# Optimization experiments

Hardware: AMD Instinct MI355X
Metric: run time of the kernel (lower is better)

The kernel has to match this reference:

```python
import jax, jax.numpy as jnp
import numpy as np

N, D, IN, HID, OUT, E = 20000, 8, 64, 128, 64, 100000
EPS = 1e-5


def _bn(h, g, b):
    # training-mode BatchNorm1d: biased batch variance, eps=1e-5
    m = h.mean(axis=0)
    v = jnp.mean((h - m) ** 2, axis=0)
    return (h - m) * jax.lax.rsqrt(v + EPS) * g + b


def setup_inputs() -> dict:
    key = jax.random.key(0)
    ks = jax.random.split(key, 12)
    x = jax.random.normal(ks[0], (N, IN), dtype=jnp.float32)
    node_ts = jax.random.uniform(ks[1], (N,), dtype=jnp.float32)
    neighbor_idx = jax.random.randint(ks[2], (N, D), 0, N, dtype=jnp.int32)
    neighbor_ts = jax.random.uniform(ks[3], (N, D), dtype=jnp.float32)
    target = jax.random.randint(ks[4], (2, E), 0, N, dtype=jnp.int32)
    neg_pairs = jax.random.randint(ks[5], (2, E), 0, N, dtype=jnp.int32)
    W1 = jax.random.normal(ks[6], (IN, HID), dtype=jnp.float32) * (1.0 / np.sqrt(IN))
    b1 = jnp.zeros((HID,), jnp.float32)
    g1 = jnp.ones((HID,), jnp.float32)
    be1 = jnp.zeros((HID,), jnp.float32)
    W2 = jax.random.normal(ks[7], (HID, OUT), dtype=jnp.float32) * (1.0 / np.sqrt(HID))
    b2 = jnp.zeros((OUT,), jnp.float32)
    g2 = jnp.ones((OUT,), jnp.float32)
    be2 = jnp.zeros((OUT,), jnp.float32)
    Wd = jax.random.normal(ks[8], (OUT, 1), dtype=jnp.float32) * (1.0 / np.sqrt(OUT))
    bd = jnp.zeros((1,), jnp.float32)
    return {"x": x, "node_ts": node_ts, "neighbor_idx": neighbor_idx,
            "neighbor_ts": neighbor_ts, "target": target, "neg_pairs": neg_pairs,
            "W1": W1, "b1": b1, "g1": g1, "be1": be1,
            "W2": W2, "b2": b2, "g2": g2, "be2": be2, "Wd": Wd, "bd": bd}


def reference(x, node_ts, neighbor_idx, neighbor_ts, target, neg_pairs,
              W1, b1, g1, be1, W2, b2, g2, be2, Wd, bd):
    n = jnp.arange(N, dtype=neighbor_idx.dtype)
    # ---- level-2 queries: every node at its own timestamp ----
    # children = D temporal-neighbor slots + self (self always valid, ts=node_ts)
    c_idx = jnp.concatenate([neighbor_idx, n[:, None]], axis=1)          # [N, D+1]
    c_ts = jnp.concatenate([neighbor_ts, node_ts[:, None]], axis=1)      # [N, D+1]
    mask2 = jnp.concatenate([neighbor_ts <= node_ts[:, None],
                             jnp.ones((N, 1), bool)], axis=1)            # [N, D+1]
    # ---- level-1 queries: each (child node, child ts) pair ----
    ci = c_idx.reshape(-1)                                               # [M]
    cts = c_ts.reshape(-1)
    gc_idx = jnp.concatenate([neighbor_idx[ci], ci[:, None]], axis=1)    # [M, D+1]
    mask1 = jnp.concatenate([neighbor_ts[ci] <= cts[:, None],
                             jnp.ones((ci.shape[0], 1), bool)], axis=1)
    # ---- layer 0: raw features of grandchildren ----
    h0 = x[gc_idx]                                                       # [M, D+1, IN]
    m1 = mask1.astype(x.dtype)
    agg1 = jnp.einsum('mk,mkf->mf', m1, h0) / m1.sum(1, keepdims=True)   # masked mean
    h1 = jax.nn.relu(_bn(agg1 @ W1 + b1, g1, be1))                       # [M, HID]
    h1 = h1.reshape(N, D + 1, HID)
    # ---- layer 2 aggregation over temporal children ----
    m2 = mask2.astype(x.dtype)
    agg2 = jnp.einsum('nk,nkf->nf', m2, h1) / m2.sum(1, keepdims=True)
    embs = jax.nn.relu(_bn(agg2 @ W2 + b2, g2, be2))                     # [N, OUT]
    # ---- HadNet link decoder + BCEWithLogits ----
    pos = (embs[target[0]] * embs[target[1]]) @ Wd + bd                  # [E, 1]
    neg = (embs[neg_pairs[0]] * embs[neg_pairs[1]]) @ Wd + bd            # [E, 1]
    preds = jnp.concatenate([pos, neg], axis=0)[:, 0]                    # [2E]
    labels = jnp.concatenate([jnp.ones((E,), x.dtype), jnp.zeros((E,), x.dtype)])
    loss = jnp.mean(jnp.maximum(preds, 0.0) - preds * labels
                    + jnp.log1p(jnp.exp(-jnp.abs(preds))))
    return loss
```

## Files before the change

kernel.cpp:

```cpp
#include <hip/hip_runtime.h>
#include <math.h>

constexpr int kN = 20000;
constexpr int kD = 8;
constexpr int kE = 100000;
constexpr int kM = kN * 9;
constexpr int kTiles1 = kM / 16;
constexpr int kTiles3 = kN / 16;
constexpr int kGroups = kN / 16;
constexpr float kEps = 1e-5f;

constexpr int S_SUM1 = 0, S_SQ1 = 128, S_SUM2 = 256, S_SQ2 = 320;

constexpr size_t OFF_MEANP = 23040000;
constexpr size_t OFF_AGG2  = 23040000;
constexpr size_t OFF_PRE2  = 28160000;
constexpr size_t OFF_EMBS  = 33280000;
constexpr size_t OFF_EMBSW = 38400000;
constexpr size_t OFF_STATS = 43520000;

typedef short short8 __attribute__((ext_vector_type(8)));
typedef float floatx4 __attribute__((ext_vector_type(4)));

__device__ __forceinline__ unsigned f2bf(float f) {
  unsigned u = __float_as_uint(f);
  u += 0x7fffu + ((u >> 16) & 1u);
  return u >> 16;
}

__global__ __launch_bounds__(256) void k0_prefix(
    const float* __restrict__ x, const int* __restrict__ nidx,
    const float* __restrict__ nts, unsigned short* __restrict__ meanp,
    float* __restrict__ stats)
{
  if (blockIdx.x == 0 && threadIdx.x < 384) stats[threadIdx.x] = 0.f;
  const int c = blockIdx.x * 4 + (threadIdx.x >> 6);
  const int lane = threadIdx.x & 63;

  float tsv[8]; int idxv[8];
#pragma unroll
  for (int j = 0; j < 8; ++j) {
    tsv[j] = nts[c * 8 + j];
    idxv[j] = nidx[c * 8 + j];
  }
  int rank[8];
#pragma unroll
  for (int j = 0; j < 8; ++j) {
    int r = 0;
#pragma unroll
    for (int j2 = 0; j2 < 8; ++j2)
      r += (tsv[j2] < tsv[j] || (tsv[j2] == tsv[j] && j2 < j)) ? 1 : 0;
    rank[j] = r;
  }
  int ord[8];
#pragma unroll
  for (int k = 0; k < 8; ++k) {
    int js = 0;
#pragma unroll
    for (int j = 0; j < 8; ++j) if (rank[j] == k) js = j;
    ord[k] = idxv[js];
  }

  float acc = x[c * 64 + lane];
  unsigned short* mp = meanp + (size_t)c * 576 + lane;
  mp[0] = (unsigned short)f2bf(acc);
#pragma unroll
  for (int k = 0; k < 8; ++k) {
    acc += x[ord[k] * 64 + lane];
    mp[(k + 1) * 64] = (unsigned short)f2bf(acc / (float)(k + 2));
  }
}

__global__ __launch_bounds__(256) void kB_rows(
    const float* __restrict__ node_ts, const int* __restrict__ nidx,
    const float* __restrict__ nts, const unsigned short* __restrict__ meanp,
    unsigned short* __restrict__ agg1)
{
  const int n = blockIdx.x * 4 + (threadIdx.x >> 6);
  const int lane = threadIdx.x & 63;
  const float tn = node_ts[n];
  const int g = lane >> 3, jj = lane & 7;
#pragma unroll
  for (int s = 0; s < 9; ++s) {
    int c; float t;
    if (s < 8) { c = nidx[n * 8 + s]; t = nts[n * 8 + s]; }
    else       { c = n;               t = tn; }
    int rank = 0;
#pragma unroll
    for (int j = 0; j < 8; ++j) rank += (nts[c * 8 + j] <= t) ? 1 : 0;
    unsigned short v = meanp[(size_t)c * 576 + rank * 64 + lane];
    int m = n * 9 + s;
    int tt = m >> 4, r = m & 15;
    agg1[tt * 1024 + g * 128 + r * 8 + jj] = v;
  }
}

__global__ __launch_bounds__(256, 3) void k1s_stats(
    const unsigned short* __restrict__ aggA,
    const float* __restrict__ W1, const float* __restrict__ b1,
    float* __restrict__ stats)
{
  __shared__ unsigned short W1T[128 * 72];
  __shared__ float redS[256][8];
  __shared__ float redQ[256][8];

  const int tid = threadIdx.x;
  const int lane = tid & 63;
  const int wave = tid >> 6;
  const int l15 = lane & 15;
  const int q = lane >> 4;

  for (int i = tid; i < 8192; i += 256) {
    int n = i >> 6, k = i & 63;
    W1T[n * 72 + k] = (unsigned short)f2bf(W1[k * 128 + n]);
  }
  __syncthreads();

  short8 bf[8][2];
#pragma unroll
  for (int c = 0; c < 8; ++c)
#pragma unroll
    for (int s = 0; s < 2; ++s)
      bf[c][s] = *(const short8*)&W1T[(c * 16 + l15) * 72 + q * 8 + s * 32];

  float b1c[8];
#pragma unroll
  for (int c = 0; c < 8; ++c) b1c[c] = b1[c * 16 + l15];

  float sum8[8], sq8[8];
#pragma unroll
  for (int c = 0; c < 8; ++c) { sum8[c] = 0.f; sq8[c] = 0.f; }

  const int gw = blockIdx.x * 4 + wave;
  const int nw = gridDim.x * 4;

  for (int t = gw; t < kTiles1; t += nw) {
    const unsigned short* ap = aggA + (size_t)t * 1024;
    short8 af0 = *(const short8*)(ap + q * 128 + l15 * 8);
    short8 af1 = *(const short8*)(ap + (4 + q) * 128 + l15 * 8);

    floatx4 acc[8];
#pragma unroll
    for (int c = 0; c < 8; ++c) {
      acc[c] = (floatx4){0.f, 0.f, 0.f, 0.f};
      acc[c] = __builtin_amdgcn_mfma_f32_16x16x32_bf16(af0, bf[c][0], acc[c], 0, 0, 0);
      acc[c] = __builtin_amdgcn_mfma_f32_16x16x32_bf16(af1, bf[c][1], acc[c], 0, 0, 0);
    }
#pragma unroll
    for (int c = 0; c < 8; ++c)
#pragma unroll
      for (int i = 0; i < 4; ++i) {
        float v = acc[c][i] + b1c[c];
        sum8[c] += v; sq8[c] += v * v;
      }
  }

  __syncthreads();
#pragma unroll
  for (int c = 0; c < 8; ++c) { redS[tid][c] = sum8[c]; redQ[tid][c] = sq8[c]; }
  __syncthreads();
  if (tid < 128) {
    int c = tid >> 4, r15 = tid & 15;
    float s = 0.f, qq = 0.f;
#pragma unroll
    for (int w = 0; w < 4; ++w)
#pragma unroll
      for (int p = 0; p < 4; ++p) {
        int T = w * 64 + p * 16 + r15;
        s += redS[T][c]; qq += redQ[T][c];
      }
    atomicAdd(&stats[S_SUM1 + tid], s);
    atomicAdd(&stats[S_SQ1 + tid], qq);
  }
}

__global__ __launch_bounds__(256, 2) void k2_apply(
    const unsigned short* __restrict__ aggA, const float* __restrict__ node_ts,
    const float* __restrict__ nts, const float* __restrict__ W1,
    const float* __restrict__ b1, const float* __restrict__ g1,
    const float* __restrict__ be1, const float* __restrict__ stats,
    unsigned* __restrict__ agg2dw)
{
  __shared__ unsigned short W1T[128 * 72];
  __shared__ unsigned short H[144 * 128];
  __shared__ float sc[128], sh[128];
  __shared__ float wbuf[144];
  __shared__ float rvs[16];

  const int tid = threadIdx.x;
  const int lane = tid & 63;
  const int wave = tid >> 6;
  const int l15 = lane & 15;
  const int q = lane >> 4;
  const int g = blockIdx.x;
  const int n0 = g * 16;

  for (int i = tid; i < 8192; i += 256) {
    int n = i >> 6, k = i & 63;
    W1T[n * 72 + k] = (unsigned short)f2bf(W1[k * 128 + n]);
  }
  if (tid < 128) {
    float mean = stats[S_SUM1 + tid] * (1.f / kM);
    float var  = stats[S_SQ1 + tid] * (1.f / kM) - mean * mean;
    float s    = g1[tid] * rsqrtf(var + kEps);
    sc[tid] = s; sh[tid] = be1[tid] - mean * s;
  }
  if (tid < 144) {
    int nd = n0 + tid / 9, slot = tid % 9;
    wbuf[tid] = (slot < kD) ? ((nts[nd * kD + slot] <= node_ts[nd]) ? 1.f : 0.f)
                            : 1.f;
  }
  __syncthreads();

  short8 bfr[8][2];
#pragma unroll
  for (int c = 0; c < 8; ++c)
#pragma unroll
    for (int s = 0; s < 2; ++s)
      bfr[c][s] = *(const short8*)&W1T[(c * 16 + l15) * 72 + q * 8 + s * 32];

  float scc[8], shc[8];
#pragma unroll
  for (int c = 0; c < 8; ++c) {
    int col = c * 16 + l15;
    scc[c] = sc[col];
    shc[c] = fmaf(b1[col], sc[col], sh[col]);
  }
  if (tid < 16) {
    float s = 0.f;
#pragma unroll
    for (int j = 0; j < 9; ++j) s += wbuf[tid * 9 + j];
    rvs[tid] = 1.f / s;
  }

  for (int t9 = wave; t9 < 9; t9 += 4) {
    const unsigned short* ap = aggA + (size_t)(g * 9 + t9) * 1024;
    short8 af0 = *(const short8*)(ap + q * 128 + l15 * 8);
    short8 af1 = *(const short8*)(ap + (4 + q) * 128 + l15 * 8);

    floatx4 acc[8];
#pragma unroll
    for (int c = 0; c < 8; ++c) {
      acc[c] = (floatx4){0.f, 0.f, 0.f, 0.f};
      acc[c] = __builtin_amdgcn_mfma_f32_16x16x32_bf16(af0, bfr[c][0], acc[c], 0, 0, 0);
      acc[c] = __builtin_amdgcn_mfma_f32_16x16x32_bf16(af1, bfr[c][1], acc[c], 0, 0, 0);
    }
#pragma unroll
    for (int i = 0; i < 4; ++i) {
      int lr = t9 * 16 + q * 4 + i;
#pragma unroll
      for (int c = 0; c < 8; ++c) {
        int col = c * 16 + l15;
        float h = fmaxf(fmaf(acc[c][i], scc[c], shc[c]), 0.f);
        H[lr * 128 + col] = (unsigned short)f2bf(h);
      }
    }
  }
  __syncthreads();

  const unsigned* Hdw = (const unsigned*)H;
#pragma unroll
  for (int j = 0; j < 4; ++j) {
    int ndl = 4 * wave + j;
    float s0 = 0.f, s1 = 0.f;
#pragma unroll
    for (int slot = 0; slot < 9; ++slot) {
      int lr = ndl * 9 + slot;
      float w = wbuf[lr];
      unsigned u = Hdw[lr * 64 + lane];
      s0 = fmaf(w, __uint_as_float(u << 16), s0);
      s1 = fmaf(w, __uint_as_float(u & 0xffff0000u), s1);
    }
    float r = rvs[ndl];
    agg2dw[(size_t)(n0 + ndl) * 64 + lane] =
        f2bf(s0 * r) | (f2bf(s1 * r) << 16);
  }
}

__global__ __launch_bounds__(256, 3) void k3b_gemm2(
    const unsigned short* __restrict__ agg2, const float* __restrict__ W2,
    const float* __restrict__ b2, float* __restrict__ stats,
    float* __restrict__ pre2)
{
  __shared__ unsigned short W2T[64 * 136];
  __shared__ float redS[256][4];
  __shared__ float redQ[256][4];

  const int tid = threadIdx.x;
  const int lane = tid & 63;
  const int wave = tid >> 6;
  const int l15 = lane & 15;
  const int q = lane >> 4;

  for (int i = tid; i < 8192; i += 256) {
    int n = i >> 7, k = i & 127;
    W2T[n * 136 + k] = (unsigned short)f2bf(W2[k * 64 + n]);
  }
  __syncthreads();

  short8 bfr[4][4];
#pragma unroll
  for (int c = 0; c < 4; ++c)
#pragma unroll
    for (int s = 0; s < 4; ++s)
      bfr[c][s] = *(const short8*)&W2T[(c * 16 + l15) * 136 + q * 8 + s * 32];

  float b2c[4];
#pragma unroll
  for (int c = 0; c < 4; ++c) b2c[c] = b2[c * 16 + l15];

  float sum4[4], sq4[4];
#pragma unroll
  for (int c = 0; c < 4; ++c) { sum4[c] = 0.f; sq4[c] = 0.f; }

  const int gw = blockIdx.x * 4 + wave;
  const int nw = gridDim.x * 4;

  for (int t = gw; t < kTiles3; t += nw) {
    const int r0 = t * 16;
    short8 af[4];
#pragma unroll
    for (int s = 0; s < 4; ++s)
      af[s] = *(const short8*)&agg2[(size_t)(r0 + l15) * 128 + q * 8 + s * 32];

    floatx4 acc[4];
#pragma unroll
    for (int c = 0; c < 4; ++c) {
      acc[c] = (floatx4){0.f, 0.f, 0.f, 0.f};
#pragma unroll
      for (int s = 0; s < 4; ++s)
        acc[c] = __builtin_amdgcn_mfma_f32_16x16x32_bf16(af[s], bfr[c][s], acc[c], 0, 0, 0);
    }
#pragma unroll
    for (int c = 0; c < 4; ++c) {
      int col = c * 16 + l15;
#pragma unroll
      for (int i = 0; i < 4; ++i) {
        float v = acc[c][i] + b2c[c];
        int row = r0 + q * 4 + i;
        pre2[(size_t)row * 64 + col] = v;
        sum4[c] += v; sq4[c] += v * v;
      }
    }
  }

  __syncthreads();
#pragma unroll
  for (int c = 0; c < 4; ++c) { redS[tid][c] = sum4[c]; redQ[tid][c] = sq4[c]; }
  __syncthreads();
  if (tid < 64) {
    int c = tid >> 4, r15 = tid & 15;
    float s = 0.f, qq = 0.f;
#pragma unroll
    for (int w = 0; w < 4; ++w)
#pragma unroll
      for (int p = 0; p < 4; ++p) {
        int T = w * 64 + p * 16 + r15;
        s += redS[T][c]; qq += redQ[T][c];
      }
    atomicAdd(&stats[S_SUM2 + tid], s);
    atomicAdd(&stats[S_SQ2 + tid], qq);
  }
}

__global__ __launch_bounds__(256) void k5_embs(
    const float* __restrict__ pre2, const float* __restrict__ stats,
    const float* __restrict__ g2, const float* __restrict__ be2,
    const float* __restrict__ Wd, float* __restrict__ embs,
    float* __restrict__ embsW, float* __restrict__ out)
{
  __shared__ float sc[64], sh[64], wd[64];
  const int tid = threadIdx.x;
  if (blockIdx.x == 0 && tid == 0) out[0] = 0.f;
  if (tid < 64) {
    float mean = stats[S_SUM2 + tid] * (1.f / kN);
    float var  = stats[S_SQ2 + tid] * (1.f / kN) - mean * mean;
    float s    = g2[tid] * rsqrtf(var + kEps);
    sc[tid] = s; sh[tid] = be2[tid] - mean * s; wd[tid] = Wd[tid];
  }
  __syncthreads();
  int idx = blockIdx.x * 256 + tid;
  int col = idx & 63;
  float e = fmaxf(fmaf(pre2[idx], sc[col], sh[col]), 0.f);
  embs[idx] = e;
  embsW[idx] = e * wd[col];
}

__global__ __launch_bounds__(256) void k6_loss(
    const float* __restrict__ embs, const float* __restrict__ embsW,
    const int* __restrict__ tgt, const int* __restrict__ neg,
    const float* __restrict__ bd, float* __restrict__ out)
{
  __shared__ float redl[256];
  const int tid = threadIdx.x;
  const int tq = tid & 15;
  const int qb = tid >> 4;
  const float bd0 = bd[0];
  float lsum = 0.f;
  const int e0 = blockIdx.x * 128 + qb * 8;
#pragma unroll
  for (int it = 0; it < 8; ++it) {
    int e = e0 + it;
    if (e < 2 * kE) {
      int i, j; float lab;
      if (e < kE) { i = tgt[e];      j = tgt[kE + e]; lab = 1.f; }
      else        { i = neg[e - kE]; j = neg[e];      lab = 0.f; }
      float4 av = *(const float4*)(embsW + (size_t)i * 64 + tq * 4);
      float4 bv = *(const float4*)(embs  + (size_t)j * 64 + tq * 4);
      float p = av.x * bv.x + av.y * bv.y + av.z * bv.z + av.w * bv.w;
      p += __shfl_xor(p, 1); p += __shfl_xor(p, 2);
      p += __shfl_xor(p, 4); p += __shfl_xor(p, 8);
      p += bd0;
      float l = fmaxf(p, 0.f) - p * lab + log1pf(expf(-fabsf(p)));
      if (tq == 0) lsum += l;
    }
  }
  redl[tid] = lsum;
  __syncthreads();
  for (int s = 128; s > 0; s >>= 1) {
    if (tid < s) redl[tid] += redl[tid + s];
    __syncthreads();
  }
  if (tid == 0) atomicAdd(out, redl[0] * (1.f / (2 * kE)));
}

extern "C" void kernel_launch(void* const* d_in, const int* in_sizes, int n_in,
                              void* d_out, int out_size, void* d_ws, size_t ws_size,
                              hipStream_t stream) {
  (void)in_sizes; (void)n_in; (void)out_size; (void)ws_size;
  const float* x       = (const float*)d_in[0];
  const float* node_ts = (const float*)d_in[1];
  const int*   nidx    = (const int*)d_in[2];
  const float* nts     = (const float*)d_in[3];
  const int*   tgt     = (const int*)d_in[4];
  const int*   neg     = (const int*)d_in[5];
  const float* W1      = (const float*)d_in[6];
  const float* b1      = (const float*)d_in[7];
  const float* g1      = (const float*)d_in[8];
  const float* be1     = (const float*)d_in[9];
  const float* W2      = (const float*)d_in[10];
  const float* b2      = (const float*)d_in[11];
  const float* g2      = (const float*)d_in[12];
  const float* be2     = (const float*)d_in[13];
  const float* Wd      = (const float*)d_in[14];
  const float* bd      = (const float*)d_in[15];

  char* ws = (char*)d_ws;
  unsigned short* agg1  = (unsigned short*)ws;
  unsigned short* meanp = (unsigned short*)(ws + OFF_MEANP);
  unsigned short* agg2  = (unsigned short*)(ws + OFF_AGG2);
  float* pre2  = (float*)(ws + OFF_PRE2);
  float* embs  = (float*)(ws + OFF_EMBS);
  float* embsW = (float*)(ws + OFF_EMBSW);
  float* stats = (float*)(ws + OFF_STATS);
  float* out   = (float*)d_out;

  k0_prefix<<<kN / 4, 256, 0, stream>>>(x, nidx, nts, meanp, stats);
  kB_rows<<<kN / 4, 256, 0, stream>>>(node_ts, nidx, nts, meanp, agg1);
  k1s_stats<<<512, 256, 0, stream>>>(agg1, W1, b1, stats);
  k2_apply<<<kGroups, 256, 0, stream>>>(agg1, node_ts, nts, W1, b1, g1, be1,
                                        stats, (unsigned*)agg2);
  k3b_gemm2<<<160, 256, 0, stream>>>(agg2, W2, b2, stats, pre2);
  k5_embs<<<kN * 64 / 256, 256, 0, stream>>>(pre2, stats, g2, be2, Wd, embs,
                                             embsW, out);
  k6_loss<<<(2 * kE + 127) / 128, 256, 0, stream>>>(embs, embsW, tgt, neg, bd, out);
}
```

Before: 228.6 us.

## Replace materialized agg1 with row-index indirection into prefix-mean table

Removes the kB_rows kernel that copied prefix-mean rows into a tiled agg1 buffer. The prep kernel now writes a per-row index (child*9 + rank), and both GEMM kernels gather their A fragments straight from the prefix-mean table through that index. This drops one launch and the write-then-read of a 23 MB bf16 intermediate. In exchange the GEMM loads become indirect, less coalesced gathers.

```diff
diff --git a/kernel.cpp b/kernel.cpp
--- a/kernel.cpp
+++ b/kernel.cpp
@@ -12,12 +12,12 @@
 
 constexpr int S_SUM1 = 0, S_SQ1 = 128, S_SUM2 = 256, S_SQ2 = 320;
 
-constexpr size_t OFF_MEANP = 23040000;
-constexpr size_t OFF_AGG2  = 23040000;
-constexpr size_t OFF_PRE2  = 28160000;
-constexpr size_t OFF_EMBS  = 33280000;
-constexpr size_t OFF_EMBSW = 38400000;
-constexpr size_t OFF_STATS = 43520000;
+constexpr size_t OFF_AGG2   = 23040000;
+constexpr size_t OFF_PRE2   = 28160000;
+constexpr size_t OFF_EMBS   = 33280000;
+constexpr size_t OFF_EMBSW  = 38400000;
+constexpr size_t OFF_STATS  = 43520000;
+constexpr size_t OFF_ROWIDX = 43524096;
 
 typedef short short8 __attribute__((ext_vector_type(8)));
 typedef float floatx4 __attribute__((ext_vector_type(4)));
@@ -28,9 +28,10 @@
   return u >> 16;
 }
 
-__global__ __launch_bounds__(256) void k0_prefix(
-    const float* __restrict__ x, const int* __restrict__ nidx,
-    const float* __restrict__ nts, unsigned short* __restrict__ meanp,
+__global__ __launch_bounds__(256) void kA_prep(
+    const float* __restrict__ x, const float* __restrict__ node_ts,
+    const int* __restrict__ nidx, const float* __restrict__ nts,
+    unsigned short* __restrict__ meanp, int* __restrict__ rowidx,
     float* __restrict__ stats)
 {
   if (blockIdx.x == 0 && threadIdx.x < 384) stats[threadIdx.x] = 0.f;
@@ -69,34 +70,25 @@
     acc += x[ord[k] * 64 + lane];
     mp[(k + 1) * 64] = (unsigned short)f2bf(acc / (float)(k + 2));
   }
-}
-
-__global__ __launch_bounds__(256) void kB_rows(
-    const float* __restrict__ node_ts, const int* __restrict__ nidx,
-    const float* __restrict__ nts, const unsigned short* __restrict__ meanp,
-    unsigned short* __restrict__ agg1)
-{
-  const int n = blockIdx.x * 4 + (threadIdx.x >> 6);
-  const int lane = threadIdx.x & 63;
-  const float tn = node_ts[n];
-  const int g = lane >> 3, jj = lane & 7;
-#pragma unroll
-  for (int s = 0; s < 9; ++s) {
-    int c; float t;
-    if (s < 8) { c = nidx[n * 8 + s]; t = nts[n * 8 + s]; }
-    else       { c = n;               t = tn; }
-    int rank = 0;
-#pragma unroll
-    for (int j = 0; j < 8; ++j) rank += (nts[c * 8 + j] <= t) ? 1 : 0;
-    unsigned short v = meanp[(size_t)c * 576 + rank * 64 + lane];
-    int m = n * 9 + s;
-    int tt = m >> 4, r = m & 15;
-    agg1[tt * 1024 + g * 128 + r * 8 + jj] = v;
+
+  if (lane < 9) {
+    int cc; float t;
+    if (lane < 8) { cc = idxv[lane]; t = tsv[lane]; }
+    else          { cc = c;          t = node_ts[c]; }
+    int r = 0;
+    if (lane < 8) {
+#pragma unroll
+      for (int j = 0; j < 8; ++j) r += (nts[cc * 8 + j] <= t) ? 1 : 0;
+    } else {
+#pragma unroll
+      for (int j = 0; j < 8; ++j) r += (tsv[j] <= t) ? 1 : 0;
+    }
+    rowidx[c * 9 + lane] = cc * 9 + r;
   }
 }
 
 __global__ __launch_bounds__(256, 3) void k1s_stats(
-    const unsigned short* __restrict__ aggA,
+    const unsigned short* __restrict__ meanp, const int* __restrict__ rowidx,
     const float* __restrict__ W1, const float* __restrict__ b1,
     float* __restrict__ stats)
 {
@@ -135,9 +127,10 @@
   const int nw = gridDim.x * 4;
 
   for (int t = gw; t < kTiles1; t += nw) {
-    const unsigned short* ap = aggA + (size_t)t * 1024;
-    short8 af0 = *(const short8*)(ap + q * 128 + l15 * 8);
-    short8 af1 = *(const short8*)(ap + (4 + q) * 128 + l15 * 8);
+    int rid = rowidx[t * 16 + l15];
+    const unsigned short* ap = meanp + (size_t)rid * 64;
+    short8 af0 = *(const short8*)(ap + q * 8);
+    short8 af1 = *(const short8*)(ap + 32 + q * 8);
 
     floatx4 acc[8];
 #pragma unroll
@@ -175,11 +168,11 @@
 }
 
 __global__ __launch_bounds__(256, 2) void k2_apply(
-    const unsigned short* __restrict__ aggA, const float* __restrict__ node_ts,
-    const float* __restrict__ nts, const float* __restrict__ W1,
-    const float* __restrict__ b1, const float* __restrict__ g1,
-    const float* __restrict__ be1, const float* __restrict__ stats,
-    unsigned* __restrict__ agg2dw)
+    const unsigned short* __restrict__ meanp, const int* __restrict__ rowidx,
+    const float* __restrict__ node_ts, const float* __restrict__ nts,
+    const float* __restrict__ W1, const float* __restrict__ b1,
+    const float* __restrict__ g1, const float* __restrict__ be1,
+    const float* __restrict__ stats, unsigned* __restrict__ agg2dw)
 {
   __shared__ unsigned short W1T[128 * 72];
   __shared__ unsigned short H[144 * 128];
@@ -234,9 +227,10 @@
   }
 
   for (int t9 = wave; t9 < 9; t9 += 4) {
-    const unsigned short* ap = aggA + (size_t)(g * 9 + t9) * 1024;
-    short8 af0 = *(const short8*)(ap + q * 128 + l15 * 8);
-    short8 af1 = *(const short8*)(ap + (4 + q) * 128 + l15 * 8);
+    int rid = rowidx[g * 144 + t9 * 16 + l15];
+    const unsigned short* ap = meanp + (size_t)rid * 64;
+    short8 af0 = *(const short8*)(ap + q * 8);
+    short8 af1 = *(const short8*)(ap + 32 + q * 8);
 
     floatx4 acc[8];
 #pragma unroll
@@ -446,20 +440,19 @@
   const float* bd      = (const float*)d_in[15];
 
   char* ws = (char*)d_ws;
-  unsigned short* agg1  = (unsigned short*)ws;
-  unsigned short* meanp = (unsigned short*)(ws + OFF_MEANP);
+  unsigned short* meanp = (unsigned short*)ws;
   unsigned short* agg2  = (unsigned short*)(ws + OFF_AGG2);
-  float* pre2  = (float*)(ws + OFF_PRE2);
-  float* embs  = (float*)(ws + OFF_EMBS);
-  float* embsW = (float*)(ws + OFF_EMBSW);
-  float* stats = (float*)(ws + OFF_STATS);
-  float* out   = (float*)d_out;
-
-  k0_prefix<<<kN / 4, 256, 0, stream>>>(x, nidx, nts, meanp, stats);
-  kB_rows<<<kN / 4, 256, 0, stream>>>(node_ts, nidx, nts, meanp, agg1);
-  k1s_stats<<<512, 256, 0, stream>>>(agg1, W1, b1, stats);
-  k2_apply<<<kGroups, 256, 0, stream>>>(agg1, node_ts, nts, W1, b1, g1, be1,
-                                        stats, (unsigned*)agg2);
+  float* pre2   = (float*)(ws + OFF_PRE2);
+  float* embs   = (float*)(ws + OFF_EMBS);
+  float* embsW  = (float*)(ws + OFF_EMBSW);
+  float* stats  = (float*)(ws + OFF_STATS);
+  int*   rowidx = (int*)(ws + OFF_ROWIDX);
+  float* out    = (float*)d_out;
+
+  kA_prep<<<kN / 4, 256, 0, stream>>>(x, node_ts, nidx, nts, meanp, rowidx, stats);
+  k1s_stats<<<512, 256, 0, stream>>>(meanp, rowidx, W1, b1, stats);
+  k2_apply<<<kGroups, 256, 0, stream>>>(meanp, rowidx, node_ts, nts, W1, b1,
+                                        g1, be1, stats, (unsigned*)agg2);
   k3b_gemm2<<<160, 256, 0, stream>>>(agg2, W2, b2, stats, pre2);
   k5_embs<<<kN * 64 / 256, 256, 0, stream>>>(pre2, stats, g2, be2, Wd, embs,
                                              embsW, out);
```

New measurement: 223.1 us. 1.02x faster.
